# Optimization experiments

Measured on AMD Instinct MI355X. Metric: run time of the kernel, lower is better.

Reference implementation:

```python
import jax, jax.numpy as jnp
import numpy as np

HIDDEN = 768
FF = 3072
N_HEADS = 12
HEAD = HIDDEN // N_HEADS
WIDTH = 512  # attention window (number of attended keys, causal)
B, S = 2, 4096
EPS = 1e-6


def _rotary_sincos(seq_len, dim):
    # GPT-J style: freqs per pair, each value repeated twice (interleaved)
    inv_freq = 1.0 / (10000.0 ** (np.arange(0, dim, 2, dtype=np.float32) / dim))
    t = np.arange(seq_len, dtype=np.float32)
    ang = np.einsum('s,d->sd', t, inv_freq)              # [S, dim/2]
    ang = np.repeat(ang, 2, axis=-1)                     # [S, dim]
    return jnp.asarray(np.sin(ang))[:, None, :], jnp.asarray(np.cos(ang))[:, None, :]


def setup_inputs() -> dict:
    key = jax.random.key(0)
    ks = jax.random.split(key, 4)
    x = jax.random.normal(ks[0], (B, S, HIDDEN), dtype=jnp.float32)
    sin, cos = _rotary_sincos(S, HEAD)                   # [S,1,HEAD] each
    W_in = jax.random.normal(ks[1], (HIDDEN, 3 * HIDDEN + FF), dtype=jnp.float32) / np.sqrt(HIDDEN)
    b_in = jnp.zeros((3 * HIDDEN + FF,), dtype=jnp.float32)
    W_out = jax.random.normal(ks[2], (HIDDEN + FF, HIDDEN), dtype=jnp.float32) / np.sqrt(HIDDEN + FF)
    b_out = jnp.zeros((HIDDEN,), dtype=jnp.float32)
    w_norm = jnp.ones((HIDDEN,), dtype=jnp.float32)
    return {"x": x, "sin": sin, "cos": cos, "w_norm": w_norm,
            "W_in": W_in, "b_in": b_in, "W_out": W_out, "b_out": b_out}


def _rotate_every_two(x):
    x1 = x[..., ::2]
    x2 = x[..., 1::2]
    return jnp.stack((-x2, x1), axis=-1).reshape(x.shape)


def _apply_rope(x, sin, cos):
    # x: [B,S,H,hd]; sin/cos: [S,1,hd] -> broadcast as [1,S,1,hd]
    sin = sin[None]
    cos = cos[None]
    return x * cos + _rotate_every_two(x) * sin


def _windowed_attention(q, k, v, width):
    # q,k,v: [B,S,H,hd]; causal local attention: key j valid iff 0 <= i-j < width
    b, s, h, d = q.shape
    wb = width  # block size == window; each query block attends blocks (b-1, b)
    nb = s // wb
    scale = 1.0 / np.sqrt(d)
    qb = q.reshape(b, nb, wb, h, d)
    kp = jnp.pad(k, ((0, 0), (wb, 0), (0, 0), (0, 0))).reshape(b, nb + 1, wb, h, d)
    vp = jnp.pad(v, ((0, 0), (wb, 0), (0, 0), (0, 0))).reshape(b, nb + 1, wb, h, d)
    kb = jnp.concatenate([kp[:, :-1], kp[:, 1:]], axis=2)   # [B,nb,2wb,H,hd]
    vb = jnp.concatenate([vp[:, :-1], vp[:, 1:]], axis=2)
    scores = jnp.einsum('bnqhd,bnkhd->bnhqk', qb, kb) * scale
    qi = jnp.arange(wb)
    ki = jnp.arange(2 * wb)
    bi = jnp.arange(nb)
    diff = wb + qi[:, None] - ki[None, :]                    # i - j per block
    base = (diff >= 0) & (diff < width)                      # [wb, 2wb]
    valid_j = (bi[:, None, None] >= 1) | (ki[None, None, :] >= wb)  # j >= 0
    mask = base[None] & valid_j                              # [nb, wb, 2wb]
    neg = jnp.finfo(scores.dtype).min
    scores = jnp.where(mask[None, :, None], scores, neg)
    p = jax.nn.softmax(scores, axis=-1)
    out = jnp.einsum('bnhqk,bnkhd->bnqhd', p, vb)
    return out.reshape(b, s, h * d)


def reference(x, sin, cos, w_norm, W_in, b_in, W_out, b_out):
    # RMSNorm
    ms = jnp.mean(x * x, axis=-1, keepdims=True)
    xn = x * jax.lax.rsqrt(ms + EPS) * w_norm
    # fused QKV + FF projection
    t = xn @ W_in + b_in                                     # [B,S,3*HIDDEN+FF]
    ff = t[:, :, -FF:]
    qkv = t[:, :, :-FF].reshape(x.shape[0], x.shape[1], 3, N_HEADS, HEAD)
    q = _apply_rope(qkv[:, :, 0], sin, cos)
    k = _apply_rope(qkv[:, :, 1], sin, cos)
    v = qkv[:, :, 2]
    attn = _windowed_attention(q, k, v, WIDTH)               # [B,S,HIDDEN]
    ff = jax.nn.gelu(ff, approximate=False)
    combined = jnp.concatenate((attn, ff), axis=-1)          # [B,S,HIDDEN+FF]
    return combined @ W_out + b_out
```

## Files before the change

kernel.cpp:

```cpp
#include <hip/hip_runtime.h>
#include <hip/hip_bf16.h>

typedef short bf16x8 __attribute__((ext_vector_type(8)));
typedef float f32x4 __attribute__((ext_vector_type(4)));

#define LOG2E 1.4426950408889634f
#define QKV_E ((size_t)24*4096*64)

__device__ __forceinline__ float bfu2f(unsigned short u) {
  unsigned v = ((unsigned)u) << 16;
  return __builtin_bit_cast(float, v);
}
__device__ __forceinline__ unsigned short f2bfu(float f) {
  unsigned u = __builtin_bit_cast(unsigned, f);
  u += 0x7fffu + ((u >> 16) & 1u);
  return (unsigned short)(u >> 16);
}
__device__ __forceinline__ unsigned packbf2(float lo, float hi) {
  return (unsigned)f2bfu(lo) | ((unsigned)f2bfu(hi) << 16);
}
__device__ __forceinline__ float gelu_f(float v) {
  float a = fabsf(v) * 0.70710678118654752f;
  float t = 1.0f / (1.0f + 0.3275911f * a);
  float poly = ((((1.061405429f * t - 1.453152027f) * t + 1.421413741f) * t
                 - 0.284496736f) * t + 0.254829592f) * t;
  float erfa = 1.0f - poly * __expf(-a * a);
  float erfv = v >= 0.0f ? erfa : -erfa;
  return 0.5f * v * (1.0f + erfv);
}
__device__ __forceinline__ void gl_lds16(const ushort* g, ushort* l) {
  __builtin_amdgcn_global_load_lds(
      (const __attribute__((address_space(1))) unsigned int*)(const void*)g,
      (__attribute__((address_space(3))) unsigned int*)(void*)l, 16, 0, 0);
}
#define WAIT_VM8  asm volatile("s_waitcnt vmcnt(8)" ::: "memory")
#define WAIT_VM0  asm volatile("s_waitcnt vmcnt(0)" ::: "memory")
#define WAIT_LGKM asm volatile("s_waitcnt lgkmcnt(0)" ::: "memory")
#define BAR       __builtin_amdgcn_s_barrier()

__global__ __launch_bounds__(256) void rmsnorm_k(const float* __restrict__ x,
    const float* __restrict__ w, ushort* __restrict__ xn) {
  int row = blockIdx.x, t = threadIdx.x;
  const float* xr = x + (size_t)row * 768;
  float v0 = xr[t], v1 = xr[t + 256], v2 = xr[t + 512];
  float ss = v0 * v0 + v1 * v1 + v2 * v2;
#pragma unroll
  for (int m = 32; m >= 1; m >>= 1) ss += __shfl_xor(ss, m, 64);
  __shared__ float part[4];
  if ((t & 63) == 0) part[t >> 6] = ss;
  __syncthreads();
  float tot = part[0] + part[1] + part[2] + part[3];
  float rr = rsqrtf(tot * (1.0f / 768.0f) + 1e-6f);
  ushort* xo = xn + (size_t)row * 768;
  xo[t]       = f2bfu(v0 * rr * w[t]);
  xo[t + 256] = f2bfu(v1 * rr * w[t + 256]);
  xo[t + 512] = f2bfu(v2 * rr * w[t + 512]);
}

__global__ __launch_bounds__(256) void tcvt_k(const float* __restrict__ in,
    ushort* __restrict__ out, int R, int C) {
  __shared__ float tile[32][33];
  int c0 = blockIdx.x * 32, r0 = blockIdx.y * 32;
  int t = threadIdx.x;
  int j = t & 31, i0 = t >> 5;
#pragma unroll
  for (int i = i0; i < 32; i += 8) tile[i][j] = in[(size_t)(r0 + i) * C + c0 + j];
  __syncthreads();
#pragma unroll
  for (int i = i0; i < 32; i += 8) out[(size_t)(c0 + i) * R + r0 + j] = f2bfu(tile[j][i]);
}

__global__ __launch_bounds__(256, 2) void gemm1_k(const ushort* __restrict__ A,
    const ushort* __restrict__ Bt, const float* __restrict__ bias,
    const float* __restrict__ sn, const float* __restrict__ cs,
    ushort* __restrict__ qbuf, ushort* __restrict__ kbuf,
    ushort* __restrict__ vt, ushort* __restrict__ comb) {
  __shared__ __align__(16) ushort lds[2][2][128 * 64];
  const int t = threadIdx.x, lane = t & 63, w = t >> 6;
  const int wr = w >> 1, wc = w & 1;
  int bid = blockIdx.x;
  int xcd = bid & 7, local = bid >> 3;
  int grp = local / 48, r6 = local % 48;
  int bx = grp * 6 + r6 % 6;
  int by = xcd * 8 + r6 / 6;
  const int mBase = by * 128, nBase = bx * 128;

  size_t gA[4], gB[4];
  int ldst[4];
#pragma unroll
  for (int j = 0; j < 4; ++j) {
    int row = w * 32 + j * 8 + (lane >> 3);
    int gc = ((lane & 7) ^ (lane >> 3)) * 8;
    gA[j] = (size_t)(mBase + row) * 768 + gc;
    gB[j] = (size_t)(nBase + row) * 768 + gc;
    ldst[j] = (w * 32 + j * 8) * 64;
  }

  f32x4 acc[4][4];
  f32x4 z = {0.f, 0.f, 0.f, 0.f};
#pragma unroll
  for (int m = 0; m < 4; ++m)
#pragma unroll
    for (int nn = 0; nn < 4; ++nn) acc[m][nn] = z;

#pragma unroll
  for (int j = 0; j < 4; ++j) {
    gl_lds16(A + gA[j], &lds[0][0][0] + ldst[j]);
    gl_lds16(Bt + gB[j], &lds[0][1][0] + ldst[j]);
  }

#pragma unroll 1
  for (int kt = 0; kt < 12; ++kt) {
    const int cur = kt & 1;
    if (kt < 11) {
      int k0 = (kt + 1) * 64;
#pragma unroll
      for (int j = 0; j < 4; ++j) {
        gl_lds16(A + gA[j] + k0, &lds[1 - cur][0][0] + ldst[j]);
        gl_lds16(Bt + gB[j] + k0, &lds[1 - cur][1][0] + ldst[j]);
      }
      WAIT_VM8;
    } else {
      WAIT_VM0;
    }
    BAR;
    const ushort* As = &lds[cur][0][0];
    const ushort* Bs = &lds[cur][1][0];
#pragma unroll
    for (int kk = 0; kk < 2; ++kk) {
      bf16x8 af[4], bff[4];
#pragma unroll
      for (int m = 0; m < 4; ++m) {
        int row = wr * 64 + m * 16 + (lane & 15);
        int slot = (kk * 4 + (lane >> 4)) ^ (lane & 7);
        af[m] = *(const bf16x8*)(As + row * 64 + slot * 8);
      }
#pragma unroll
      for (int nn = 0; nn < 4; ++nn) {
        int row = wc * 64 + nn * 16 + (lane & 15);
        int slot = (kk * 4 + (lane >> 4)) ^ (lane & 7);
        bff[nn] = *(const bf16x8*)(Bs + row * 64 + slot * 8);
      }
#pragma unroll
      for (int m = 0; m < 4; ++m)
#pragma unroll
        for (int nn = 0; nn < 4; ++nn)
          acc[m][nn] = __builtin_amdgcn_mfma_f32_16x16x32_bf16(bff[nn], af[m], acc[m][nn], 0, 0, 0);
    }
    WAIT_LGKM;
    BAR;
  }

  const bool isff = (nBase >= 2304);
  const int region = nBase / 768;
#pragma unroll
  for (int m = 0; m < 4; ++m) {
    int row = mBase + wr * 64 + m * 16 + (lane & 15);
    int b = row >> 12, s = row & 4095;
#pragma unroll
    for (int nn = 0; nn < 4; ++nn) {
      int col = nBase + wc * 64 + nn * 16 + ((lane >> 4) << 2);
      f32x4 v = acc[m][nn] + *(const f32x4*)(bias + col);
      if (isff) {
        ushort4 o;
        o.x = f2bfu(gelu_f(v[0]));
        o.y = f2bfu(gelu_f(v[1]));
        o.z = f2bfu(gelu_f(v[2]));
        o.w = f2bfu(gelu_f(v[3]));
        *(ushort4*)(comb + (size_t)row * 3840 + (col - 1536)) = o;
      } else {
        int rem = col - region * 768;
        int h = rem >> 6, d0 = rem & 63;
        if (region == 2) {
          int l = s & 127;
          int pnn = l >> 4, pg = (l >> 2) & 3, pr = l & 3;
          int sp = (s & ~127) | (((pnn >> 1) * 4 + pg) * 8 + (pnn & 1) * 4 + pr);
          size_t vb = (size_t)((b * 12 + h) * 64 + d0) * 4096 + sp;
          vt[vb]          = f2bfu(v[0]);
          vt[vb + 4096]   = f2bfu(v[1]);
          vt[vb + 2*4096] = f2bfu(v[2]);
          vt[vb + 3*4096] = f2bfu(v[3]);
        } else {
          f32x4 sv = *(const f32x4*)(sn + (s << 6) + d0);
          f32x4 cv = *(const f32x4*)(cs + (s << 6) + d0);
          float o0 = v[0] * cv[0] - v[1] * sv[0];
          float o1 = v[1] * cv[0] + v[0] * sv[0];
          float o2 = v[2] * cv[2] - v[3] * sv[2];
          float o3 = v[3] * cv[2] + v[2] * sv[2];
          ushort4 o;
          if (region == 0) {
            o.x = f2bfu(o0 * 0.125f); o.y = f2bfu(o1 * 0.125f);
            o.z = f2bfu(o2 * 0.125f); o.w = f2bfu(o3 * 0.125f);
            *(ushort4*)(qbuf + ((size_t)((b * 12 + h) * 4096 + s)) * 64 + d0) = o;
          } else {
            o.x = f2bfu(o0); o.y = f2bfu(o1); o.z = f2bfu(o2); o.w = f2bfu(o3);
            *(ushort4*)(kbuf + ((size_t)((b * 12 + h) * 4096 + s)) * 64 + d0) = o;
          }
        }
      }
    }
  }
}

__global__ __launch_bounds__(256, 2) void gemm2_k(const ushort* __restrict__ A,
    const ushort* __restrict__ Bt, const float* __restrict__ bias,
    float* __restrict__ out) {
  __shared__ __align__(16) ushort lds[2][2][128 * 64];
  const int t = threadIdx.x, lane = t & 63, w = t >> 6;
  const int wr = w >> 1, wc = w & 1;
  int bid = blockIdx.x;
  int xcd = bid & 7, local = bid >> 3;
  int g = local / 4, r4 = local % 4;
  int bx = (g % 3) * 2 + (r4 & 1);
  int by = xcd * 8 + (g / 3) * 2 + (r4 >> 1);
  const int mBase = by * 128, nBase = bx * 128;

  size_t gA[4], gB[4];
  int ldst[4];
#pragma unroll
  for (int j = 0; j < 4; ++j) {
    int row = w * 32 + j * 8 + (lane >> 3);
    int gc = ((lane & 7) ^ (lane >> 3)) * 8;
    gA[j] = (size_t)(mBase + row) * 3840 + gc;
    gB[j] = (size_t)(nBase + row) * 3840 + gc;
    ldst[j] = (w * 32 + j * 8) * 64;
  }

  f32x4 acc[4][4];
  f32x4 z = {0.f, 0.f, 0.f, 0.f};
#pragma unroll
  for (int m = 0; m < 4; ++m)
#pragma unroll
    for (int nn = 0; nn < 4; ++nn) acc[m][nn] = z;

#pragma unroll
  for (int j = 0; j < 4; ++j) {
    gl_lds16(A + gA[j], &lds[0][0][0] + ldst[j]);
    gl_lds16(Bt + gB[j], &lds[0][1][0] + ldst[j]);
  }

#pragma unroll 1
  for (int kt = 0; kt < 60; ++kt) {
    const int cur = kt & 1;
    if (kt < 59) {
      int k0 = (kt + 1) * 64;
#pragma unroll
      for (int j = 0; j < 4; ++j) {
        gl_lds16(A + gA[j] + k0, &lds[1 - cur][0][0] + ldst[j]);
        gl_lds16(Bt + gB[j] + k0, &lds[1 - cur][1][0] + ldst[j]);
      }
      WAIT_VM8;
    } else {
      WAIT_VM0;
    }
    BAR;
    const ushort* As = &lds[cur][0][0];
    const ushort* Bs = &lds[cur][1][0];
#pragma unroll
    for (int kk = 0; kk < 2; ++kk) {
      bf16x8 af[4], bff[4];
#pragma unroll
      for (int m = 0; m < 4; ++m) {
        int row = wr * 64 + m * 16 + (lane & 15);
        int slot = (kk * 4 + (lane >> 4)) ^ (lane & 7);
        af[m] = *(const bf16x8*)(As + row * 64 + slot * 8);
      }
#pragma unroll
      for (int nn = 0; nn < 4; ++nn) {
        int row = wc * 64 + nn * 16 + (lane & 15);
        int slot = (kk * 4 + (lane >> 4)) ^ (lane & 7);
        bff[nn] = *(const bf16x8*)(Bs + row * 64 + slot * 8);
      }
#pragma unroll
      for (int m = 0; m < 4; ++m)
#pragma unroll
        for (int nn = 0; nn < 4; ++nn)
          acc[m][nn] = __builtin_amdgcn_mfma_f32_16x16x32_bf16(bff[nn], af[m], acc[m][nn], 0, 0, 0);
    }
    WAIT_LGKM;
    BAR;
  }

#pragma unroll
  for (int m = 0; m < 4; ++m) {
    int row = mBase + wr * 64 + m * 16 + (lane & 15);
#pragma unroll
    for (int nn = 0; nn < 4; ++nn) {
      int col = nBase + wc * 64 + nn * 16 + ((lane >> 4) << 2);
      f32x4 v = acc[m][nn] + *(const f32x4*)(bias + col);
      *(f32x4*)(out + (size_t)row * 768 + col) = v;
    }
  }
}

__global__ __launch_bounds__(256, 2) void attn_k(const ushort* __restrict__ qb,
    const ushort* __restrict__ kb, const ushort* __restrict__ vt,
    ushort* __restrict__ comb) {
  __shared__ __align__(16) ushort KS[2][128 * 64];
  __shared__ __align__(16) ushort VS[2][64 * 128];
  int bid = blockIdx.x;
  int nb = (bid & 7) * 96 + (bid >> 3);
  int qt = nb & 31, bh = nb >> 5;
  const int t = threadIdx.x, lane = t & 63, w = t >> 6;
  const int g = lane >> 4, q15 = lane & 15;
  const int qlo = qt * 128;
  const size_t base = (size_t)bh * 4096 * 64;

  size_t kSrc[4], vSrc[4];
  int dstOff[4];
#pragma unroll
  for (int j = 0; j < 4; ++j) {
    int ck = (w * 4 + j) * 64 + lane;
    int key = ck >> 3, sl = ck & 7;
    kSrc[j] = (size_t)key * 64 + ((sl ^ (key & 7)) << 3);
    int dd = ck >> 4, s16 = ck & 15;
    vSrc[j] = (size_t)dd * 4096 + ((s16 ^ (dd & 15)) << 3);
    dstOff[j] = (w * 4 + j) * 512;
  }

  bf16x8 qa[2][2];
#pragma unroll
  for (int m = 0; m < 2; ++m)
#pragma unroll
    for (int kk = 0; kk < 2; ++kk) {
      int row = qlo + w * 32 + m * 16 + q15;
      qa[m][kk] = *(const bf16x8*)(qb + base + (size_t)row * 64 + kk * 32 + g * 8);
    }

  f32x4 z = {0.f, 0.f, 0.f, 0.f};
  f32x4 o[2][4];
#pragma unroll
  for (int m = 0; m < 2; ++m)
#pragma unroll
    for (int df = 0; df < 4; ++df) o[m][df] = z;
  float m_run[2] = {-1e30f, -1e30f}, l_run[2] = {0.f, 0.f};

  const int t0 = qt >= 4 ? qt - 4 : 0;
  const int nt = qt - t0 + 1;
  {
    int k0 = t0 * 128;
#pragma unroll
    for (int j = 0; j < 4; ++j) {
      gl_lds16(kb + base + (size_t)k0 * 64 + kSrc[j], &KS[0][0] + dstOff[j]);
      gl_lds16(vt + base + k0 + vSrc[j], &VS[0][0] + dstOff[j]);
    }
  }

  const int qrow0 = qlo + w * 32 + q15;
#pragma unroll 1
  for (int it = 0; it < nt; ++it) {
    const int kt = t0 + it, k0 = kt * 128, cur = it & 1;
    if (it + 1 < nt) {
      int k1 = k0 + 128;
#pragma unroll
      for (int j = 0; j < 4; ++j) {
        gl_lds16(kb + base + (size_t)k1 * 64 + kSrc[j], &KS[1 - cur][0] + dstOff[j]);
        gl_lds16(vt + base + k1 + vSrc[j], &VS[1 - cur][0] + dstOff[j]);
      }
      WAIT_VM8;
    } else {
      WAIT_VM0;
    }
    BAR;
    f32x4 s[2][8];
#pragma unroll
    for (int m = 0; m < 2; ++m)
#pragma unroll
      for (int nn = 0; nn < 8; ++nn) s[m][nn] = z;
#pragma unroll
    for (int kk = 0; kk < 2; ++kk) {
      bf16x8 kf[8];
#pragma unroll
      for (int nn = 0; nn < 8; ++nn) {
        int row = nn * 16 + q15;
        int slot = (kk * 4 + g) ^ (q15 & 7);
        kf[nn] = *(const bf16x8*)(&KS[cur][0] + row * 64 + slot * 8);
      }
#pragma unroll
      for (int m = 0; m < 2; ++m)
#pragma unroll
        for (int nn = 0; nn < 8; ++nn)
          s[m][nn] = __builtin_amdgcn_mfma_f32_16x16x32_bf16(kf[nn], qa[m][kk], s[m][nn], 0, 0, 0);
    }
    if (kt == qt) {
#pragma unroll
      for (int m = 0; m < 2; ++m) {
        int ql = qrow0 + m * 16 - k0;
#pragma unroll
        for (int nn = 0; nn < 8; ++nn)
#pragma unroll
          for (int r = 0; r < 4; ++r)
            if (nn * 16 + g * 4 + r > ql) s[m][nn][r] = -3e38f;
      }
    } else if (kt == qt - 4) {
#pragma unroll
      for (int m = 0; m < 2; ++m) {
        int ql = qrow0 + m * 16 - k0;
#pragma unroll
        for (int nn = 0; nn < 8; ++nn)
#pragma unroll
          for (int r = 0; r < 4; ++r)
            if (ql - (nn * 16 + g * 4 + r) >= 512) s[m][nn][r] = -3e38f;
      }
    }
    float mx[2];
    bool need = false;
#pragma unroll
    for (int m = 0; m < 2; ++m) {
      float v = s[m][0][0];
#pragma unroll
      for (int nn = 0; nn < 8; ++nn)
#pragma unroll
        for (int r = 0; r < 4; ++r) v = fmaxf(v, s[m][nn][r]);
      v = fmaxf(v, __shfl_xor(v, 16, 64));
      v = fmaxf(v, __shfl_xor(v, 32, 64));
      mx[m] = v;
      need |= (v > m_run[m] + 8.f);
    }
    if (__any(need)) {
#pragma unroll
      for (int m = 0; m < 2; ++m) {
        float mn = fmaxf(m_run[m], mx[m]);
        float sc = exp2f((m_run[m] - mn) * LOG2E);
        m_run[m] = mn;
        l_run[m] *= sc;
#pragma unroll
        for (int df = 0; df < 4; ++df) o[m][df] *= sc;
      }
    }
#pragma unroll
    for (int m = 0; m < 2; ++m) {
      float mr = m_run[m];
      float ls = 0.f;
#pragma unroll
      for (int nn = 0; nn < 8; ++nn)
#pragma unroll
        for (int r = 0; r < 4; ++r) {
          float p = exp2f((s[m][nn][r] - mr) * LOG2E);
          s[m][nn][r] = p;
          ls += p;
        }
      ls += __shfl_xor(ls, 16, 64);
      ls += __shfl_xor(ls, 32, 64);
      l_run[m] += ls;
    }
#pragma unroll
    for (int kk2 = 0; kk2 < 4; ++kk2) {
      bf16x8 pa[2];
#pragma unroll
      for (int m = 0; m < 2; ++m) {
        int4 pi4;
        pi4.x = (int)packbf2(s[m][2*kk2][0],   s[m][2*kk2][1]);
        pi4.y = (int)packbf2(s[m][2*kk2][2],   s[m][2*kk2][3]);
        pi4.z = (int)packbf2(s[m][2*kk2+1][0], s[m][2*kk2+1][1]);
        pi4.w = (int)packbf2(s[m][2*kk2+1][2], s[m][2*kk2+1][3]);
        pa[m] = __builtin_bit_cast(bf16x8, pi4);
      }
#pragma unroll
      for (int df = 0; df < 4; ++df) {
        int row = df * 16 + q15;
        int slot = (kk2 * 4 + g) ^ q15;
        bf16x8 vf = *(const bf16x8*)(&VS[cur][0] + row * 128 + slot * 8);
#pragma unroll
        for (int m = 0; m < 2; ++m)
          o[m][df] = __builtin_amdgcn_mfma_f32_16x16x32_bf16(vf, pa[m], o[m][df], 0, 0, 0);
      }
    }
    WAIT_LGKM;
    BAR;
  }

  int b = bh / 12, h = bh % 12;
#pragma unroll
  for (int m = 0; m < 2; ++m) {
    float inv = 1.0f / l_run[m];
    int row = qrow0 + m * 16;
#pragma unroll
    for (int df = 0; df < 4; ++df) {
      ushort4 ov;
      ov.x = f2bfu(o[m][df][0] * inv);
      ov.y = f2bfu(o[m][df][1] * inv);
      ov.z = f2bfu(o[m][df][2] * inv);
      ov.w = f2bfu(o[m][df][3] * inv);
      *(ushort4*)(comb + (size_t)(b * 4096 + row) * 3840 + h * 64 + df * 16 + g * 4) = ov;
    }
  }
}

extern "C" void kernel_launch(void* const* d_in, const int* in_sizes, int n_in,
                              void* d_out, int out_size, void* d_ws, size_t ws_size,
                              hipStream_t stream) {
  (void)in_sizes; (void)n_in; (void)out_size; (void)ws_size;
  const float* x      = (const float*)d_in[0];
  const float* sin_t  = (const float*)d_in[1];
  const float* cos_t  = (const float*)d_in[2];
  const float* w_norm = (const float*)d_in[3];
  const float* W_in   = (const float*)d_in[4];
  const float* b_in   = (const float*)d_in[5];
  const float* W_out  = (const float*)d_in[6];
  const float* b_out  = (const float*)d_in[7];
  float* out = (float*)d_out;

  const size_t XN_E  = (size_t)8192 * 768;
  ushort* xn      = (ushort*)d_ws;
  ushort* qbuf    = xn + XN_E;
  ushort* kbuf    = qbuf + QKV_E;
  ushort* vt      = kbuf + QKV_E;
  ushort* w_in_t  = vt + QKV_E;
  ushort* w_out_t = w_in_t + (size_t)5376 * 768;
  ushort* comb    = w_out_t + (size_t)768 * 3840;

  rmsnorm_k<<<dim3(8192), dim3(256), 0, stream>>>(x, w_norm, xn);
  tcvt_k<<<dim3(5376 / 32, 768 / 32), dim3(256), 0, stream>>>(W_in, w_in_t, 768, 5376);
  tcvt_k<<<dim3(768 / 32, 3840 / 32), dim3(256), 0, stream>>>(W_out, w_out_t, 3840, 768);
  gemm1_k<<<dim3(2688), dim3(256), 0, stream>>>(xn, w_in_t, b_in, sin_t, cos_t,
                                                qbuf, kbuf, vt, comb);
  attn_k<<<dim3(768), dim3(256), 0, stream>>>(qbuf, kbuf, vt, comb);
  gemm2_k<<<dim3(384), dim3(256), 0, stream>>>(comb, w_out_t, b_out, out);
}
```

Measured before the change: 238.9 us.

## Enlarge gemm1 tile to 256x256 with 8 waves and interleaved prefetch

The first GEMM moves from 128x128 tiles with 4 waves to 256x256 tiles with 8 waves (2x4 wave grid, each wave doing 128x64). The next K-tile's global-to-LDS loads are split across four sub-phases, interleaved with the MFMA groups, and s_setprio is raised around the MFMA bursts. This cuts global/LDS traffic per FLOP and overlaps loads with compute. In exchange it uses more registers (32 accumulators per wave), doubles LDS to 128KB, adds extra barriers, and leaves 672 blocks on 256 CUs, which may hurt occupancy and wave balance.

```diff
diff --git a/kernel.cpp b/kernel.cpp
--- a/kernel.cpp
+++ b/kernel.cpp
@@ -34,6 +34,7 @@
       (__attribute__((address_space(3))) unsigned int*)(void*)l, 16, 0, 0);
 }
 #define WAIT_VM8  asm volatile("s_waitcnt vmcnt(8)" ::: "memory")
+#define WAIT_VM2  asm volatile("s_waitcnt vmcnt(2)" ::: "memory")
 #define WAIT_VM0  asm volatile("s_waitcnt vmcnt(0)" ::: "memory")
 #define WAIT_LGKM asm volatile("s_waitcnt lgkmcnt(0)" ::: "memory")
 #define BAR       __builtin_amdgcn_s_barrier()
@@ -70,97 +71,99 @@
   for (int i = i0; i < 32; i += 8) out[(size_t)(c0 + i) * R + r0 + j] = f2bfu(tile[j][i]);
 }
 
-__global__ __launch_bounds__(256, 2) void gemm1_k(const ushort* __restrict__ A,
+__global__ __launch_bounds__(512, 2) void gemm1_k(const ushort* __restrict__ A,
     const ushort* __restrict__ Bt, const float* __restrict__ bias,
     const float* __restrict__ sn, const float* __restrict__ cs,
     ushort* __restrict__ qbuf, ushort* __restrict__ kbuf,
     ushort* __restrict__ vt, ushort* __restrict__ comb) {
-  __shared__ __align__(16) ushort lds[2][2][128 * 64];
+  __shared__ __align__(16) ushort lds[2][32768];
   const int t = threadIdx.x, lane = t & 63, w = t >> 6;
-  const int wr = w >> 1, wc = w & 1;
+  const int wm = w >> 2, wn = w & 3;
+  const int g = lane >> 4, q15 = lane & 15;
   int bid = blockIdx.x;
   int xcd = bid & 7, local = bid >> 3;
-  int grp = local / 48, r6 = local % 48;
-  int bx = grp * 6 + r6 % 6;
-  int by = xcd * 8 + r6 / 6;
-  const int mBase = by * 128, nBase = bx * 128;
-
-  size_t gA[4], gB[4];
-  int ldst[4];
-#pragma unroll
-  for (int j = 0; j < 4; ++j) {
-    int row = w * 32 + j * 8 + (lane >> 3);
-    int gc = ((lane & 7) ^ (lane >> 3)) * 8;
-    gA[j] = (size_t)(mBase + row) * 768 + gc;
-    gB[j] = (size_t)(nBase + row) * 768 + gc;
-    ldst[j] = (w * 32 + j * 8) * 64;
-  }
-
-  f32x4 acc[4][4];
+  int grp = local / 28, r28 = local % 28;
+  int bx = grp * 7 + r28 % 7;
+  int by = xcd * 4 + r28 / 7;
+  const int mBase = by * 256, nBase = bx * 256;
+
+  const int schk = ((t & 7) ^ ((t >> 3) & 7)) * 8;
+  const ushort* gA = A  + (size_t)(mBase + (t >> 3)) * 768 + schk;
+  const ushort* gB = Bt + (size_t)(nBase + (t >> 3)) * 768 + schk;
+  const int dstBase = w * 512;
+
+  f32x4 acc[8][4];
   f32x4 z = {0.f, 0.f, 0.f, 0.f};
 #pragma unroll
-  for (int m = 0; m < 4; ++m)
-#pragma unroll
-    for (int nn = 0; nn < 4; ++nn) acc[m][nn] = z;
-
-#pragma unroll
-  for (int j = 0; j < 4; ++j) {
-    gl_lds16(A + gA[j], &lds[0][0][0] + ldst[j]);
-    gl_lds16(Bt + gB[j], &lds[0][1][0] + ldst[j]);
+  for (int mi = 0; mi < 8; ++mi)
+#pragma unroll
+    for (int nj = 0; nj < 4; ++nj) acc[mi][nj] = z;
+
+#pragma unroll
+  for (int rd = 0; rd < 4; ++rd) {
+    gl_lds16(gA + rd * 49152, &lds[0][rd * 4096 + dstBase]);
+    gl_lds16(gB + rd * 49152, &lds[0][16384 + rd * 4096 + dstBase]);
   }
 
 #pragma unroll 1
   for (int kt = 0; kt < 12; ++kt) {
     const int cur = kt & 1;
-    if (kt < 11) {
-      int k0 = (kt + 1) * 64;
-#pragma unroll
-      for (int j = 0; j < 4; ++j) {
-        gl_lds16(A + gA[j] + k0, &lds[1 - cur][0][0] + ldst[j]);
-        gl_lds16(Bt + gB[j] + k0, &lds[1 - cur][1][0] + ldst[j]);
-      }
-      WAIT_VM8;
-    } else {
-      WAIT_VM0;
-    }
-    BAR;
-    const ushort* As = &lds[cur][0][0];
-    const ushort* Bs = &lds[cur][1][0];
-#pragma unroll
-    for (int kk = 0; kk < 2; ++kk) {
-      bf16x8 af[4], bff[4];
-#pragma unroll
-      for (int m = 0; m < 4; ++m) {
-        int row = wr * 64 + m * 16 + (lane & 15);
-        int slot = (kk * 4 + (lane >> 4)) ^ (lane & 7);
-        af[m] = *(const bf16x8*)(As + row * 64 + slot * 8);
-      }
-#pragma unroll
-      for (int nn = 0; nn < 4; ++nn) {
-        int row = wc * 64 + nn * 16 + (lane & 15);
-        int slot = (kk * 4 + (lane >> 4)) ^ (lane & 7);
-        bff[nn] = *(const bf16x8*)(Bs + row * 64 + slot * 8);
-      }
-#pragma unroll
-      for (int m = 0; m < 4; ++m)
-#pragma unroll
-        for (int nn = 0; nn < 4; ++nn)
-          acc[m][nn] = __builtin_amdgcn_mfma_f32_16x16x32_bf16(bff[nn], af[m], acc[m][nn], 0, 0, 0);
-    }
-    WAIT_LGKM;
-    BAR;
-  }
-
-  const bool isff = (nBase >= 2304);
-  const int region = nBase / 768;
-#pragma unroll
-  for (int m = 0; m < 4; ++m) {
-    int row = mBase + wr * 64 + m * 16 + (lane & 15);
+    const ushort* As = &lds[cur][0];
+    const ushort* Bs = &lds[cur][16384];
+    bf16x8 bff[4];
+#pragma unroll
+    for (int p = 0; p < 4; ++p) {
+      if (kt < 11) {
+        const int k1 = (kt + 1) * 64;
+        const int r0 = 2 * p, r1 = 2 * p + 1;
+        if (r0 < 4) gl_lds16(gA + r0 * 49152 + k1, &lds[1 - cur][r0 * 4096 + dstBase]);
+        else        gl_lds16(gB + (r0 - 4) * 49152 + k1, &lds[1 - cur][16384 + (r0 - 4) * 4096 + dstBase]);
+        if (r1 < 4) gl_lds16(gA + r1 * 49152 + k1, &lds[1 - cur][r1 * 4096 + dstBase]);
+        else        gl_lds16(gB + (r1 - 4) * 49152 + k1, &lds[1 - cur][16384 + (r1 - 4) * 4096 + dstBase]);
+      }
+      if (p == 0) {
+        if (kt < 11) { WAIT_VM2; } else { WAIT_VM0; }
+        BAR;
+      }
+      const int kk = p >> 1, mih = p & 1;
+      if (mih == 0) {
+#pragma unroll
+        for (int nj = 0; nj < 4; ++nj) {
+          int rl = wn * 64 + nj * 16 + q15;
+          bff[nj] = *(const bf16x8*)(Bs + rl * 64 + (((kk * 4 + g) ^ (q15 & 7)) << 3));
+        }
+      }
+      bf16x8 af[4];
+#pragma unroll
+      for (int i = 0; i < 4; ++i) {
+        int rl = wm * 128 + (mih * 4 + i) * 16 + q15;
+        af[i] = *(const bf16x8*)(As + rl * 64 + (((kk * 4 + g) ^ (q15 & 7)) << 3));
+      }
+      BAR;
+      __builtin_amdgcn_s_setprio(1);
+#pragma unroll
+      for (int i = 0; i < 4; ++i)
+#pragma unroll
+        for (int nj = 0; nj < 4; ++nj)
+          acc[mih * 4 + i][nj] = __builtin_amdgcn_mfma_f32_16x16x32_bf16(
+              bff[nj], af[i], acc[mih * 4 + i][nj], 0, 0, 0);
+      __builtin_amdgcn_s_setprio(0);
+      WAIT_LGKM;
+      BAR;
+    }
+  }
+
+  const int colB = nBase + wn * 64;
+  const bool isff = (colB >= 2304);
+  const int region = colB / 768;
+#pragma unroll
+  for (int mi = 0; mi < 8; ++mi) {
+    int row = mBase + wm * 128 + mi * 16 + q15;
     int b = row >> 12, s = row & 4095;
 #pragma unroll
-    for (int nn = 0; nn < 4; ++nn) {
-      int col = nBase + wc * 64 + nn * 16 + ((lane >> 4) << 2);
-      f32x4 v = acc[m][nn] + *(const f32x4*)(bias + col);
+    for (int nj = 0; nj < 4; ++nj) {
+      int col = colB + nj * 16 + g * 4;
+      f32x4 v = acc[mi][nj] + *(const f32x4*)(bias + col);
       if (isff) {
         ushort4 o;
         o.x = f2bfu(gelu_f(v[0]));
@@ -513,8 +516,8 @@
   rmsnorm_k<<<dim3(8192), dim3(256), 0, stream>>>(x, w_norm, xn);
   tcvt_k<<<dim3(5376 / 32, 768 / 32), dim3(256), 0, stream>>>(W_in, w_in_t, 768, 5376);
   tcvt_k<<<dim3(768 / 32, 3840 / 32), dim3(256), 0, stream>>>(W_out, w_out_t, 3840, 768);
-  gemm1_k<<<dim3(2688), dim3(256), 0, stream>>>(xn, w_in_t, b_in, sin_t, cos_t,
-                                                qbuf, kbuf, vt, comb);
+  gemm1_k<<<dim3(672), dim3(512), 0, stream>>>(xn, w_in_t, b_in, sin_t, cos_t,
+                                               qbuf, kbuf, vt, comb);
   attn_k<<<dim3(768), dim3(256), 0, stream>>>(qbuf, kbuf, vt, comb);
   gemm2_k<<<dim3(384), dim3(256), 0, stream>>>(comb, w_out_t, b_out, out);
 }
```

Result: no change. 234.8 us (-1.7%).
